# Kernel tuning notes

Measured on AMD Instinct MI355X. Metric: run time of the kernel, lower is better.

Reference implementation:

```python
import jax, jax.numpy as jnp
import numpy as np
from jax import lax

PAD_ID = 0
V, E = 100000, 300          # word vocab / embedding dim
VC, EC, C = 100, 50, 100    # char vocab / char emb dim / char conv channels
H, L = 256, 17              # lstm hidden / n_labels
B, S, LC = 32, 128, 50


def _conv1d(x, w, b):
    # x [B, Cin, T], w [Cout, Cin, K] -> valid conv
    y = lax.conv_general_dilated(x, w, window_strides=(1,), padding='VALID',
                                 dimension_numbers=('NCH', 'OIH', 'NCH'))
    return y + b[None, :, None]


def _lstm_dir(x_sbd, w_ih, w_hh, b, h0, c0):
    # x_sbd [S,B,D]; PyTorch gate order i,f,g,o
    def step(carry, x_t):
        h, c = carry
        g = x_t @ w_ih.T + h @ w_hh.T + b
        i, f, gg, o = jnp.split(g, 4, axis=-1)
        c = jax.nn.sigmoid(f) * c + jax.nn.sigmoid(i) * jnp.tanh(gg)
        h = jax.nn.sigmoid(o) * jnp.tanh(c)
        return (h, c), h
    _, hs = lax.scan(step, (h0, c0), x_sbd)
    return hs  # [S,B,H]


def _emissions(x, x_char, word_emb, char_emb,
               conv1_w, conv1_b, conv2_w, conv2_b, conv3_w, conv3_b,
               w_ih_f, w_hh_f, b_f, w_ih_b, w_hh_b, b_b, h0, c0, fc_w, fc_b):
    emb = word_emb[x]                                   # [B,S,E]
    ce = char_emb[x_char].transpose(0, 2, 1)            # [B,EC,LC]
    ce = jax.nn.relu(_conv1d(ce, conv1_w, conv1_b))
    ce = jax.nn.relu(_conv1d(ce, conv2_w, conv2_b))
    ce = jax.nn.relu(_conv1d(ce, conv3_w, conv3_b))
    pooled = ce.max(axis=2)                             # [B,C] (max over time)
    char_rep = jnp.broadcast_to(pooled[:, None, :], (emb.shape[0], emb.shape[1], pooled.shape[1]))
    xin = jnp.concatenate([emb, char_rep], axis=2)      # [B,S,E+C]
    xs = xin.transpose(1, 0, 2)                         # [S,B,D]
    hf = _lstm_dir(xs, w_ih_f, w_hh_f, b_f, h0[0], c0[0])
    hb = _lstm_dir(xs[::-1], w_ih_b, w_hh_b, b_b, h0[1], c0[1])[::-1]
    hcat = jnp.concatenate([hf, hb], axis=-1).transpose(1, 0, 2)  # [B,S,2H]
    em = hcat @ fc_w.T + fc_b                           # [B,S,L]
    return jax.nn.softmax(em, axis=1)                   # faithful: softmax over seq dim


def _viterbi(emissions, mask, start_t, trans, end_t):
    # emissions [B,S,L], mask [B,S]
    em = emissions.transpose(1, 0, 2)                   # [S,B,L]
    m = mask.T                                          # [S,B]
    score0 = start_t[None, :] + em[0]                   # [B,L]

    def fwd(score, inp):
        e_t, m_t = inp
        cand = score[:, :, None] + trans[None] + e_t[:, None, :]  # [B,L,L]
        nscore = cand.max(axis=1)
        idx = cand.argmax(axis=1).astype(jnp.int32)
        score = jnp.where(m_t[:, None] > 0, nscore, score)
        return score, idx

    score, hist = lax.scan(fwd, score0, (em[1:], m[1:]))  # hist [S-1,B,L]
    score = score + end_t[None, :]
    last = jnp.argmax(score, axis=-1).astype(jnp.int32)   # [B]

    def back(cur, inp):
        h_t, m_t = inp
        prev = jnp.take_along_axis(h_t, cur[:, None], axis=1)[:, 0]
        cur = jnp.where(m_t > 0, prev, cur)
        return cur, cur

    _, tags_rev = lax.scan(back, last, (hist[::-1], m[1:][::-1]))
    tags = jnp.concatenate([tags_rev[::-1], last[None]], axis=0)  # [S,B]
    return tags.T                                                 # [B,S]


def setup_inputs() -> dict:
    key = jax.random.key(0)
    ks = jax.random.split(key, 24)
    f = lambda i, shape, s=0.1: (jax.random.normal(ks[i], shape, dtype=jnp.float32) * s)
    inp = {
        'x': jax.random.randint(ks[0], (B, S), 1, V),          # no PAD -> mask all ones
        'x_char': jax.random.randint(ks[1], (B, LC), 1, VC),
        'word_emb': f(2, (V, E), 1.0),
        'char_emb': f(3, (VC, EC), 1.0).at[PAD_ID].set(0.0),
        'conv1_w': f(4, (C, EC, 3)), 'conv1_b': f(5, (C,)),
        'conv2_w': f(6, (C, C, 4)), 'conv2_b': f(7, (C,)),
        'conv3_w': f(8, (C, C, 5)), 'conv3_b': f(9, (C,)),
        'w_ih_f': f(10, (4 * H, E + C)), 'w_hh_f': f(11, (4 * H, H)), 'b_f': f(12, (4 * H,)),
        'w_ih_b': f(13, (4 * H, E + C)), 'w_hh_b': f(14, (4 * H, H)), 'b_b': f(15, (4 * H,)),
        'h0': f(16, (2, B, H), 1.0), 'c0': f(17, (2, B, H), 1.0),
        'fc_w': f(18, (L, 2 * H)), 'fc_b': f(19, (L,)),
        'start_t': f(20, (L,)), 'trans': f(21, (L, L)), 'end_t': f(22, (L,)),
    }
    return inp


def reference(x, x_char, word_emb, char_emb, conv1_w, conv1_b, conv2_w, conv2_b,
              conv3_w, conv3_b, w_ih_f, w_hh_f, b_f, w_ih_b, w_hh_b, b_b,
              h0, c0, fc_w, fc_b, start_t, trans, end_t):
    mask = (x != PAD_ID).astype(jnp.float32)
    em = _emissions(x, x_char, word_emb, char_emb, conv1_w, conv1_b, conv2_w, conv2_b,
                    conv3_w, conv3_b, w_ih_f, w_hh_f, b_f, w_ih_b, w_hh_b, b_b,
                    h0, c0, fc_w, fc_b)
    return _viterbi(em, mask, start_t, trans, end_t)
```

## Files before the change

### kernel.cpp

```cpp
#include <hip/hip_runtime.h>
#include <cmath>

#define B_   32
#define S_   128
#define E_   300
#define C_   100
#define EC_  50
#define LC_  50
#define H_   256
#define G4_  1024
#define L_   17
#define DHID_ 400
#define SLAB_ 8192
#define SENT2_ 0x7E007E00u
#define KP_   208

#define MRB_HINIT 0
#define MNB_HINIT 256
#define MRB_PW    256
#define MNB_PW    64
#define MRB_PB1   320
#define MNB_PB1   128
#define NBLK_MISC 448

#define TRB_FC   0
#define TNB_FC   128
#define TRB_SMV  128
#define TNB_SMV  32
#define NBLK_TAIL 160
#define F_EM  6

typedef _Float16 half8 __attribute__((ext_vector_type(8)));
typedef float f32x4 __attribute__((ext_vector_type(4)));
typedef unsigned long long ull;
struct __align__(16) U2 { ull x, y; };

__device__ __forceinline__ unsigned pack_split(float v) {
  _Float16 hi = (fabsf(v) >= 6.104e-5f) ? (_Float16)v : (_Float16)0.0f;
  float hif = (float)hi;
  _Float16 lo = (_Float16)((v - hif) * 2048.0f);
  return (unsigned)__builtin_bit_cast(unsigned short, hi)
       | ((unsigned)__builtin_bit_cast(unsigned short, lo) << 16);
}

__device__ __forceinline__ void flag_signal(int* f) {
  __syncthreads();
  if (threadIdx.x == 0)
    __hip_atomic_fetch_add(f, 1, __ATOMIC_RELEASE, __HIP_MEMORY_SCOPE_AGENT);
}
__device__ __forceinline__ void flag_wait(const int* f, int target) {
  while (__hip_atomic_load(f, __ATOMIC_ACQUIRE, __HIP_MEMORY_SCOPE_AGENT) < target)
    __builtin_amdgcn_s_sleep(16);
}

__global__ void k_misc(const int* __restrict__ x, const float* __restrict__ word_emb,
                       const float* __restrict__ h0,
                       const float* __restrict__ w_ih_f, const float* __restrict__ w_ih_b,
                       unsigned* __restrict__ hfrag,
                       unsigned* __restrict__ apH, unsigned* __restrict__ apL,
                       unsigned* __restrict__ bpH, unsigned* __restrict__ bpL,
                       int* __restrict__ flags) {
  const int bid = blockIdx.x;
  const int tid = threadIdx.x;
  if (bid == 0 && tid < 128) flags[tid] = 0;

  if (bid < MRB_PW) {
    const int g0 = bid * 256 + tid;
    const int nth = MNB_HINIT * 256;
    const int htot = 2 * (S_ + 1) * SLAB_;
    for (int idx = g0; idx < htot; idx += nth) {
      int sd = idx / SLAB_;
      int within = idx % SLAB_;
      int t = sd % (S_ + 1), d = sd / (S_ + 1);
      if (t != 0) { hfrag[idx] = SENT2_; continue; }
      int m8 = within & 7;
      int lane = (within >> 3) & 63;
      int q = within >> 9;
      int Kt = q & 7, Nt = q >> 3;
      int m = m8 & 3, isLo = m8 >> 2;
      int k0 = Kt * 32 + (lane >> 4) * 8 + 2 * m;
      int b = Nt * 16 + (lane & 15);
      unsigned p0 = pack_split(h0[((size_t)d * B_ + b) * H_ + k0]);
      unsigned p1 = pack_split(h0[((size_t)d * B_ + b) * H_ + k0 + 1]);
      unsigned hiw = (p0 & 0xFFFFu) | (p1 << 16);
      unsigned low = (p0 >> 16) | (p1 & 0xFFFF0000u);
      hfrag[idx] = isLo ? low : hiw;
    }
    return;
  } else if (bid < MRB_PB1) {
    const int q = bid - MRB_PW;
    const int total = 2 * G4_ * KP_;
    for (int idx = q * 256 + tid; idx < total; idx += MNB_PW * 256) {
      int d = idx / (G4_ * KP_);
      int rem = idx % (G4_ * KP_);
      int j = rem / KP_, k2 = rem % KP_;
      const float* w2 = d ? w_ih_b : w_ih_f;
      float v0 = 0.f, v1 = 0.f;
      if (k2 < 200) { v0 = w2[(size_t)j * DHID_ + 2 * k2]; v1 = w2[(size_t)j * DHID_ + 2 * k2 + 1]; }
      unsigned p0 = pack_split(v0), p1 = pack_split(v1);
      apH[idx] = (p0 & 0xFFFFu) | (p1 << 16);
      apL[idx] = (p0 >> 16) | (p1 & 0xFFFF0000u);
    }
    return;
  } else {
    const int q = bid - MRB_PB1;
    if (tid < KP_) {
      int k2 = tid;
      for (int rr = 0; rr < 32; ++rr) {
        int r = q * 32 + rr;
        int t2 = r >> 5, b2 = r & 31;
        if (k2 < 150) {
          const float* e2 = word_emb + (size_t)x[b2 * S_ + t2] * E_;
          unsigned p0 = pack_split(e2[2 * k2]), p1 = pack_split(e2[2 * k2 + 1]);
          bpH[(size_t)r * KP_ + k2] = (p0 & 0xFFFFu) | (p1 << 16);
          bpL[(size_t)r * KP_ + k2] = (p0 >> 16) | (p1 & 0xFFFF0000u);
        } else if (k2 >= 200) {
          bpH[(size_t)r * KP_ + k2] = 0u;
          bpL[(size_t)r * KP_ + k2] = 0u;
        }
      }
    }
    return;
  }
}

__global__ void k_conv1(const int* __restrict__ x_char, const float* __restrict__ char_emb,
                        const float* __restrict__ w1, const float* __restrict__ b1,
                        float* __restrict__ out1) {
  int b = blockIdx.x;
  int ot = blockIdx.y;
  __shared__ float ce[EC_ * 52];
  __shared__ float wl[50 * 150];
  __shared__ int ids[LC_];
  int tid = threadIdx.x;
  if (tid < LC_) ids[tid] = x_char[b * LC_ + tid];
  __syncthreads();
  for (int idx = tid; idx < LC_ * EC_; idx += 256) {
    int t = idx / EC_, ec = idx % EC_;
    ce[ec * 52 + t] = char_emb[ids[t] * EC_ + ec];
  }
  int obase = ot * 50;
  for (int idx = tid; idx < 50 * 150; idx += 256)
    wl[idx] = w1[obase * 150 + idx];
  __syncthreads();
  for (int idx = tid; idx < 50 * 48; idx += 256) {
    int o = idx / 48, t = idx % 48;
    float acc = b1[obase + o];
    const float* wr = &wl[o * 150];
    for (int c = 0; c < EC_; ++c) {
      const float* ip = &ce[c * 52 + t];
      acc += wr[c * 3 + 0] * ip[0] + wr[c * 3 + 1] * ip[1] + wr[c * 3 + 2] * ip[2];
    }
    out1[((size_t)b * C_ + obase + o) * 48 + t] = fmaxf(acc, 0.0f);
  }
}

__global__ void k_conv2(const float* __restrict__ in, const float* __restrict__ w2,
                        const float* __restrict__ b2, float* __restrict__ out2) {
  int b = blockIdx.x, ot = blockIdx.y;
  __shared__ float il[C_ * 48];
  __shared__ float wl[25 * 400];
  int tid = threadIdx.x;
  for (int idx = tid; idx < C_ * 48; idx += 256) il[idx] = in[(size_t)b * C_ * 48 + idx];
  int obase = ot * 25;
  for (int idx = tid; idx < 25 * 400; idx += 256) wl[idx] = w2[obase * 400 + idx];
  __syncthreads();
  for (int idx = tid; idx < 25 * 45; idx += 256) {
    int o = idx / 45, t = idx % 45;
    float acc = b2[obase + o];
    const float* wr = &wl[o * 400];
    for (int c = 0; c < C_; ++c) {
      const float* ip = &il[c * 48 + t];
      acc += wr[c * 4 + 0] * ip[0] + wr[c * 4 + 1] * ip[1] +
             wr[c * 4 + 2] * ip[2] + wr[c * 4 + 3] * ip[3];
    }
    out2[((size_t)b * C_ + obase + o) * 45 + t] = fmaxf(acc, 0.0f);
  }
}

__global__ void k_conv3(const float* __restrict__ in, const float* __restrict__ w3,
                        const float* __restrict__ b3, float* __restrict__ pooled) {
  int b = blockIdx.x, ot = blockIdx.y;
  __shared__ float il[C_ * 45];
  __shared__ float wl[20 * 500];
  __shared__ float o3[20 * 44];
  int tid = threadIdx.x;
  for (int idx = tid; idx < C_ * 45; idx += 256) il[idx] = in[(size_t)b * C_ * 45 + idx];
  int obase = ot * 20;
  for (int idx = tid; idx < 20 * 500; idx += 256) wl[idx] = w3[obase * 500 + idx];
  __syncthreads();
  for (int idx = tid; idx < 20 * 41; idx += 256) {
    int o = idx / 41, t = idx % 41;
    float acc = b3[obase + o];
    const float* wr = &wl[o * 500];
    for (int c = 0; c < C_; ++c) {
      const float* ip = &il[c * 45 + t];
      acc += wr[c * 5 + 0] * ip[0] + wr[c * 5 + 1] * ip[1] + wr[c * 5 + 2] * ip[2] +
             wr[c * 5 + 3] * ip[3] + wr[c * 5 + 4] * ip[4];
    }
    o3[o * 44 + t] = fmaxf(acc, 0.0f);
  }
  __syncthreads();
  if (tid < 20) {
    float m = o3[tid * 44];
    for (int t = 1; t < 41; ++t) m = fmaxf(m, o3[tid * 44 + t]);
    pooled[b * C_ + obase + tid] = m;
  }
}

__global__ void k_pb2(const float* __restrict__ pooled,
                      unsigned* __restrict__ bpH, unsigned* __restrict__ bpL) {
  const int q = blockIdx.x;
  const int k2 = threadIdx.x;
  if (k2 < 150 || k2 >= 200) return;
  for (int rr = 0; rr < 32; ++rr) {
    int r = q * 32 + rr;
    int b2 = r & 31;
    float v0 = pooled[b2 * C_ + 2 * k2 - 300];
    float v1 = pooled[b2 * C_ + 2 * k2 - 299];
    unsigned p0 = pack_split(v0), p1 = pack_split(v1);
    bpH[(size_t)r * KP_ + k2] = (p0 & 0xFFFFu) | (p1 << 16);
    bpL[(size_t)r * KP_ + k2] = (p0 >> 16) | (p1 & 0xFFFF0000u);
  }
}

__global__ __launch_bounds__(256) void k_gemm(
    const unsigned* __restrict__ apH, const unsigned* __restrict__ apL,
    const unsigned* __restrict__ bpH, const unsigned* __restrict__ bpL,
    const float* __restrict__ b_f, const float* __restrict__ b_b,
    float* __restrict__ gi) {
  const int jt = blockIdx.x, rt = blockIdx.y, d = blockIdx.z;
  const int j0 = jt * 128, r0 = rt * 128;
  const int tid = threadIdx.x;
  const int w = tid >> 6, l = tid & 63;
  const int lx = l & 15, lq = l >> 4;

  __shared__ unsigned aH[2048], aL[2048], bH[2048], bL[2048];

  f32x4 acch[2][8], accl[2][8];
#pragma unroll
  for (int mt = 0; mt < 2; ++mt)
#pragma unroll
    for (int nt = 0; nt < 8; ++nt) {
      f32x4 z = {0.f, 0.f, 0.f, 0.f};
      acch[mt][nt] = z; accl[mt][nt] = z;
    }

  const int jr = tid >> 1, hh = tid & 1;
  const int q_st = jr >> 4, lane_lo = jr & 15;
  const unsigned* arH = apH + ((size_t)(d * G4_ + j0 + jr)) * KP_ + hh * 8;
  const unsigned* arL = apL + ((size_t)(d * G4_ + j0 + jr)) * KP_ + hh * 8;
  const unsigned* brH = bpH + ((size_t)(r0 + jr)) * KP_ + hh * 8;
  const unsigned* brL = bpL + ((size_t)(r0 + jr)) * KP_ + hh * 8;
  const int w0 = (q_st * 64 + lane_lo + 32 * hh) * 4;
  const int w1 = (q_st * 64 + lane_lo + 32 * hh + 16) * 4;

  for (int Kt = 0; Kt < 13; ++Kt) {
    uint4 a0 = *(const uint4*)(arH + Kt * 16);
    uint4 a1 = *(const uint4*)(arH + Kt * 16 + 4);
    uint4 c0v = *(const uint4*)(arL + Kt * 16);
    uint4 c1v = *(const uint4*)(arL + Kt * 16 + 4);
    uint4 e0 = *(const uint4*)(brH + Kt * 16);
    uint4 e1 = *(const uint4*)(brH + Kt * 16 + 4);
    uint4 f0 = *(const uint4*)(brL + Kt * 16);
    uint4 f1 = *(const uint4*)(brL + Kt * 16 + 4);
    *(uint4*)&aH[w0] = a0; *(uint4*)&aH[w1] = a1;
    *(uint4*)&aL[w0] = c0v; *(uint4*)&aL[w1] = c1v;
    *(uint4*)&bH[w0] = e0; *(uint4*)&bH[w1] = e1;
    *(uint4*)&bL[w0] = f0; *(uint4*)&bL[w1] = f1;
    __syncthreads();

    union u4h { uint4 u; half8 h; };
    u4h AH0, AH1, AL0, AL1;
    AH0.u = *(const uint4*)&aH[((2 * w + 0) * 64 + l) * 4];
    AH1.u = *(const uint4*)&aH[((2 * w + 1) * 64 + l) * 4];
    AL0.u = *(const uint4*)&aL[((2 * w + 0) * 64 + l) * 4];
    AL1.u = *(const uint4*)&aL[((2 * w + 1) * 64 + l) * 4];
#pragma unroll
    for (int nt = 0; nt < 8; ++nt) {
      u4h BHn, BLn;
      BHn.u = *(const uint4*)&bH[(nt * 64 + l) * 4];
      BLn.u = *(const uint4*)&bL[(nt * 64 + l) * 4];
      acch[0][nt] = __builtin_amdgcn_mfma_f32_16x16x32_f16(AH0.h, BHn.h, acch[0][nt], 0, 0, 0);
      accl[0][nt] = __builtin_amdgcn_mfma_f32_16x16x32_f16(AH0.h, BLn.h, accl[0][nt], 0, 0, 0);
      accl[0][nt] = __builtin_amdgcn_mfma_f32_16x16x32_f16(AL0.h, BHn.h, accl[0][nt], 0, 0, 0);
      acch[1][nt] = __builtin_amdgcn_mfma_f32_16x16x32_f16(AH1.h, BHn.h, acch[1][nt], 0, 0, 0);
      accl[1][nt] = __builtin_amdgcn_mfma_f32_16x16x32_f16(AH1.h, BLn.h, accl[1][nt], 0, 0, 0);
      accl[1][nt] = __builtin_amdgcn_mfma_f32_16x16x32_f16(AL1.h, BHn.h, accl[1][nt], 0, 0, 0);
    }
    __syncthreads();
  }

  const float* bias = d ? b_b : b_f;
  const float inv2048 = 1.0f / 2048.0f;
#pragma unroll
  for (int mt = 0; mt < 2; ++mt) {
#pragma unroll
    for (int nt = 0; nt < 8; ++nt) {
      int rr = r0 + nt * 16 + lx;
      int tt = rr >> 5, bb = rr & 31;
      float* dst = gi + ((size_t)(d * S_ + tt) * G4_) * B_ + bb;
#pragma unroll
      for (int r4 = 0; r4 < 4; ++r4) {
        int j = j0 + (2 * w + mt) * 16 + lq * 4 + r4;
        dst[(size_t)j * B_] = acch[mt][nt][r4] + accl[mt][nt][r4] * inv2048 + bias[j];
      }
    }
  }
}

__global__ __launch_bounds__(256, 1) void k_lstm(
    const float* __restrict__ w_hh_f, const float* __restrict__ w_hh_b,
    const float* __restrict__ c0, const float* __restrict__ gi,
    float* __restrict__ hbuf, unsigned* __restrict__ hfrag) {
  const int iblk = blockIdx.x;
  const int d = blockIdx.y;
  const int Ktown = iblk >> 1;
  const int half = iblk & 1;
  const float* whh = d ? w_hh_b : w_hh_f;
  const int tid = threadIdx.x;
  const int w = tid >> 6;
  const int l = tid & 63;
  const int lx = l & 15, lq = l >> 4;
  const int u0 = iblk * 16;

  __shared__ ull slh[2048];
  __shared__ ull sll[2048];
  __shared__ float gl[4 * 16 * 33];
  __shared__ unsigned ps[2 * 576];

  half8 whi[8], wlo[8];
#pragma unroll
  for (int Kt = 0; Kt < 8; ++Kt) {
    int row = w * H_ + u0 + lx;
    int kk0 = Kt * 32 + lq * 8;
    const float* src = whh + (size_t)row * H_ + kk0;
    float4 f0 = *(const float4*)src;
    float4 f1 = *(const float4*)(src + 4);
    float wv[8] = {f0.x, f0.y, f0.z, f0.w, f1.x, f1.y, f1.z, f1.w};
    union { unsigned short s2[8]; half8 h; } HI, LO;
#pragma unroll
    for (int j = 0; j < 8; ++j) {
      float v = wv[j];
      _Float16 hi = (fabsf(v) >= 6.104e-5f) ? (_Float16)v : (_Float16)0.0f;
      float hif = (float)hi;
      _Float16 lo = (_Float16)((v - hif) * 2048.0f);
      HI.s2[j] = __builtin_bit_cast(unsigned short, hi);
      LO.s2[j] = __builtin_bit_cast(unsigned short, lo);
    }
    whi[Kt] = HI.h;
    wlo[Kt] = LO.h;
  }

  const int bc = tid & 31, cw = tid >> 5;
  float creg[2];
#pragma unroll
  for (int cu = 0; cu < 2; ++cu)
    creg[cu] = c0[((size_t)d * B_ + bc) * H_ + u0 + cu * 8 + cw];

  const int pNt = bc >> 4;
  const int pm = cw >> 1;
  const bool phi = (cw & 1) == 0;
  const int plane = bc & 15;
  const float inv2048 = 1.0f / 2048.0f;

  for (int t = 0; t < S_; ++t) {
    int torig = d ? (S_ - 1 - t) : t;

    f32x4 acch[2], accl[2];
    {
      const float* gbase = gi + ((size_t)(d * S_ + torig) * G4_) * B_;
#pragma unroll
      for (int Nt = 0; Nt < 2; ++Nt) {
        f32x4 v;
#pragma unroll
        for (int r = 0; r < 4; ++r) {
          int j = w * H_ + u0 + lq * 4 + r;
          v[r] = gbase[(size_t)j * B_ + Nt * 16 + lx];
        }
        acch[Nt] = v;
        f32x4 z = {0.f, 0.f, 0.f, 0.f};
        accl[Nt] = z;
      }
    }

    const ull* hp = (const ull*)(hfrag + (size_t)(d * (S_ + 1) + t) * SLAB_);
    ull pv[4][4];
#pragma unroll
    for (int c = 0; c < 4; ++c) {
      size_t base = ((size_t)(w * 4 + c) * 64 + l) * 4;
#pragma unroll
      for (int j = 0; j < 4; ++j)
        pv[c][j] = __hip_atomic_load(&hp[base + j], __ATOMIC_RELAXED,
                                     __HIP_MEMORY_SCOPE_AGENT);
    }
    for (;;) {
      bool pending = false;
#pragma unroll
      for (int c = 0; c < 4; ++c)
#pragma unroll
        for (int j = 0; j < 4; ++j)
          pending |= ((unsigned)pv[c][j] == SENT2_) |
                     ((unsigned)(pv[c][j] >> 32) == SENT2_);
      if (!pending) break;
#pragma unroll
      for (int c = 0; c < 4; ++c) {
        size_t base = ((size_t)(w * 4 + c) * 64 + l) * 4;
#pragma unroll
        for (int j = 0; j < 4; ++j)
          pv[c][j] = __hip_atomic_load(&hp[base + j], __ATOMIC_RELAXED,
                                       __HIP_MEMORY_SCOPE_AGENT);
      }
    }
#pragma unroll
    for (int c = 0; c < 4; ++c) {
      int idx = ((w * 4 + c) * 64 + l) * 2;
      U2 vh; vh.x = pv[c][0]; vh.y = pv[c][1];
      U2 vl; vl.x = pv[c][2]; vl.y = pv[c][3];
      *(U2*)&slh[idx] = vh;
      *(U2*)&sll[idx] = vl;
    }
    __syncthreads();

#pragma unroll
    for (int Kt = 0; Kt < 8; ++Kt) {
      half8 Bhi[2], Blo[2];
#pragma unroll
      for (int Nt = 0; Nt < 2; ++Nt) {
        int idx = ((Nt * 8 + Kt) * 64 + l) * 2;
        union { U2 u; half8 h; } UH, UL;
        UH.u = *(const U2*)&slh[idx];
        UL.u = *(const U2*)&sll[idx];
        Bhi[Nt] = UH.h;
        Blo[Nt] = UL.h;
      }
#pragma unroll
      for (int Nt = 0; Nt < 2; ++Nt) {
        acch[Nt] = __builtin_amdgcn_mfma_f32_16x16x32_f16(whi[Kt], Bhi[Nt], acch[Nt], 0, 0, 0);
        accl[Nt] = __builtin_amdgcn_mfma_f32_16x16x32_f16(whi[Kt], Blo[Nt], accl[Nt], 0, 0, 0);
        accl[Nt] = __builtin_amdgcn_mfma_f32_16x16x32_f16(wlo[Kt], Bhi[Nt], accl[Nt], 0, 0, 0);
      }
    }

#pragma unroll
    for (int Nt = 0; Nt < 2; ++Nt)
#pragma unroll
      for (int r = 0; r < 4; ++r) {
        int ul = lq * 4 + r;
        gl[(w * 16 + ul) * 33 + Nt * 16 + lx] = acch[Nt][r] + accl[Nt][r] * inv2048;
      }
    __syncthreads();

    float hreg[2];
#pragma unroll
    for (int cu = 0; cu < 2; ++cu) {
      int u = cu * 8 + cw;
      float g_i = gl[(0 * 16 + u) * 33 + bc];
      float g_f = gl[(1 * 16 + u) * 33 + bc];
      float g_g = gl[(2 * 16 + u) * 33 + bc];
      float g_o = gl[(3 * 16 + u) * 33 + bc];
      float si = 1.f / (1.f + __expf(-g_i));
      float sf = 1.f / (1.f + __expf(-g_f));
      float so = 1.f / (1.f + __expf(-g_o));
      float tg = 1.f - 2.f / (__expf(2.f * g_g) + 1.f);
      float cn = sf * creg[cu] + si * tg;
      float tc = 1.f - 2.f / (__expf(2.f * cn) + 1.f);
      float hn = so * tc;
      creg[cu] = cn;
      hreg[cu] = hn;
      unsigned me = pack_split(hn);
      unsigned pa = (unsigned)__shfl_xor((int)me, 32, 64);
      unsigned je = (cw & 1) ? pa : me;
      unsigned jo = (cw & 1) ? me : pa;
      unsigned hiw = (je & 0xFFFFu) | (jo << 16);
      unsigned low = (je >> 16) | (jo & 0xFFFF0000u);
      int lane2g = ((half * 2 + cu) << 4) | plane;
      int m8 = phi ? pm : (4 + pm);
      ps[pNt * 576 + lane2g * 9 + m8] = phi ? hiw : low;
    }
    __syncthreads();

    {
      ull* slab64 = (ull*)(hfrag + (size_t)(d * (S_ + 1) + t + 1) * SLAB_);
      int Nt = tid >> 7;
      int r = tid & 127;
      int lane2g = half * 32 + (r >> 2);
      int m2 = r & 3;
      unsigned a = ps[Nt * 576 + lane2g * 9 + 2 * m2];
      unsigned b2 = ps[Nt * 576 + lane2g * 9 + 2 * m2 + 1];
      ull v = (ull)a | ((ull)b2 << 32);
      __hip_atomic_store(&slab64[(size_t)(Nt * 8 + Ktown) * 256 + (size_t)half * 128 + r], v,
                         __ATOMIC_RELAXED, __HIP_MEMORY_SCOPE_AGENT);
      float* hb = hbuf + (size_t)(d * (S_ + 1) + t + 1) * (H_ * B_) + u0 * B_;
      hb[0 * 256 + tid] = hreg[0];
      hb[1 * 256 + tid] = hreg[1];
    }
  }
}

__global__ __launch_bounds__(256) void k_tail(
    const int* __restrict__ x, const float* __restrict__ hbuf,
    const float* __restrict__ fc_w, const float* __restrict__ fc_b,
    const float* __restrict__ start_t, const float* __restrict__ trans,
    const float* __restrict__ end_t,
    float* __restrict__ em, int* __restrict__ flags, int* __restrict__ out) {
  const int bid = blockIdx.x;
  union SMemTail {
    struct { float wT[512 * 18]; float psum[256 * 18]; } fc;
    struct { float e[S_ * L_]; float tr[L_ * L_]; float sc[2][L_];
             int hist[(S_ - 1) * L_]; int tags[S_]; } smv;
  };
  __shared__ SMemTail sm;

  if (bid < TRB_SMV) {
    const int s = bid;
    const int tid = threadIdx.x;
    float* wT = sm.fc.wT;
    float* psum = sm.fc.psum;
    for (int i = tid; i < L_ * 512; i += 256) {
      int l2 = i / 512, k = i % 512;
      wT[k * 18 + l2] = fc_w[i];
    }
    __syncthreads();
    const int b2 = tid & 31, kq = tid >> 5;
    const float* hf = hbuf + (size_t)(s + 1) * (H_ * B_);
    const float* hbk = hbuf + (size_t)(S_ + 1 + (S_ - s)) * (H_ * B_);
    float acc[L_];
#pragma unroll
    for (int l2 = 0; l2 < L_; ++l2) acc[l2] = 0.f;
    for (int i = 0; i < 64; ++i) {
      int k = kq * 64 + i;
      float hv = (k < 256) ? hf[k * 32 + b2] : hbk[(k - 256) * 32 + b2];
      const float* wr = &wT[k * 18];
#pragma unroll
      for (int l2 = 0; l2 < L_; ++l2) acc[l2] = fmaf(hv, wr[l2], acc[l2]);
    }
#pragma unroll
    for (int l2 = 0; l2 < L_; ++l2) psum[tid * 18 + l2] = acc[l2];
    __syncthreads();
    for (int idx = tid; idx < B_ * L_; idx += 256) {
      int bb2 = idx & 31, l2 = idx >> 5;
      float sum = fc_b[l2];
      for (int q2 = 0; q2 < 8; ++q2) sum += psum[(q2 * 32 + bb2) * 18 + l2];
      em[((size_t)bb2 * S_ + s) * L_ + l2] = sum;
    }
    flag_signal(&flags[F_EM]);
    return;
  } else {
    const int bb = bid - TRB_SMV;
    const int tid = threadIdx.x;
    float* e = sm.smv.e;
    float* tr = sm.smv.tr;
    auto sc = sm.smv.sc;
    int* hist = sm.smv.hist;
    int* tags = sm.smv.tags;

    if (tid == 0) flag_wait(&flags[F_EM], TNB_FC);
    __syncthreads();
    for (int i = tid; i < S_ * L_; i += 256) e[i] = em[(size_t)bb * S_ * L_ + i];
    for (int i = tid; i < L_ * L_; i += 256) tr[i] = trans[i];
    __syncthreads();
    if (tid < L_) {
      int l2 = tid;
      float m = -INFINITY;
      for (int s2 = 0; s2 < S_; ++s2) m = fmaxf(m, e[s2 * L_ + l2]);
      float sum2 = 0.f;
      for (int s2 = 0; s2 < S_; ++s2) {
        float ex = expf(e[s2 * L_ + l2] - m);
        e[s2 * L_ + l2] = ex;
        sum2 += ex;
      }
      for (int s2 = 0; s2 < S_; ++s2) e[s2 * L_ + l2] = e[s2 * L_ + l2] / sum2;
    }
    __syncthreads();
    if (tid < L_) sc[0][tid] = start_t[tid] + e[tid];
    __syncthreads();
    int cbuf = 0;
    for (int t2 = 1; t2 < S_; ++t2) {
      if (tid < L_) {
        int j2 = tid;
        float evv = e[t2 * L_ + j2];
        float best = -INFINITY;
        int arg = 0;
        for (int i = 0; i < L_; ++i) {
          float v = (sc[cbuf][i] + tr[i * L_ + j2]) + evv;
          if (v > best) { best = v; arg = i; }
        }
        int maskt = (x[bb * S_ + t2] != 0);
        sc[cbuf ^ 1][j2] = maskt ? best : sc[cbuf][j2];
        hist[(t2 - 1) * L_ + j2] = arg;
      }
      __syncthreads();
      cbuf ^= 1;
    }
    if (tid == 0) {
      float best = -INFINITY;
      int last = 0;
      for (int j2 = 0; j2 < L_; ++j2) {
        float v = sc[cbuf][j2] + end_t[j2];
        if (v > best) { best = v; last = j2; }
      }
      int cur = last;
      tags[S_ - 1] = cur;
      for (int p = S_ - 2; p >= 0; --p) {
        if (x[bb * S_ + p + 1] != 0) cur = hist[p * L_ + cur];
        tags[p] = cur;
      }
    }
    __syncthreads();
    for (int s2 = tid; s2 < S_; s2 += 256) out[bb * S_ + s2] = tags[s2];
    return;
  }
}

extern "C" void kernel_launch(void* const* d_in, const int* in_sizes, int n_in,
                              void* d_out, int out_size, void* d_ws, size_t ws_size,
                              hipStream_t stream) {
  const int* x        = (const int*)d_in[0];
  const int* x_char   = (const int*)d_in[1];
  const float* word_emb = (const float*)d_in[2];
  const float* char_emb = (const float*)d_in[3];
  const float* conv1_w = (const float*)d_in[4];
  const float* conv1_b = (const float*)d_in[5];
  const float* conv2_w = (const float*)d_in[6];
  const float* conv2_b = (const float*)d_in[7];
  const float* conv3_w = (const float*)d_in[8];
  const float* conv3_b = (const float*)d_in[9];
  const float* w_ih_f = (const float*)d_in[10];
  const float* w_hh_f = (const float*)d_in[11];
  const float* b_f    = (const float*)d_in[12];
  const float* w_ih_b = (const float*)d_in[13];
  const float* w_hh_b = (const float*)d_in[14];
  const float* b_b    = (const float*)d_in[15];
  const float* h0     = (const float*)d_in[16];
  const float* c0     = (const float*)d_in[17];
  const float* fc_w   = (const float*)d_in[18];
  const float* fc_b   = (const float*)d_in[19];
  const float* start_t = (const float*)d_in[20];
  const float* trans  = (const float*)d_in[21];
  const float* end_t  = (const float*)d_in[22];
  int* out = (int*)d_out;

  char* ws = (char*)d_ws;
  auto alloc = [&](size_t bytes) -> char* {
    char* p = ws;
    ws += (bytes + 1023) & ~(size_t)1023;
    return p;
  };
  float* pooled  = (float*)alloc(sizeof(float) * B_ * C_);
  float* gi      = (float*)alloc(sizeof(float) * 2 * S_ * G4_ * B_);
  float* hbuf    = (float*)alloc(sizeof(float) * 2 * (S_ + 1) * H_ * B_);
  unsigned* hfrag = (unsigned*)alloc(sizeof(unsigned) * 2 * (S_ + 1) * SLAB_);
  unsigned* apH  = (unsigned*)alloc(sizeof(unsigned) * 2 * G4_ * KP_);
  unsigned* apL  = (unsigned*)alloc(sizeof(unsigned) * 2 * G4_ * KP_);
  unsigned* bpH  = (unsigned*)alloc(sizeof(unsigned) * 4096 * KP_);
  unsigned* bpL  = (unsigned*)alloc(sizeof(unsigned) * 4096 * KP_);
  float* out1    = (float*)alloc(sizeof(float) * B_ * C_ * 48);
  float* out2    = (float*)alloc(sizeof(float) * B_ * C_ * 45);
  float* em      = (float*)alloc(sizeof(float) * B_ * S_ * L_);
  int* flags     = (int*)alloc(sizeof(int) * 128);

  k_misc<<<NBLK_MISC, 256, 0, stream>>>(x, word_emb, h0, w_ih_f, w_ih_b,
                                        hfrag, apH, apL, bpH, bpL, flags);
  k_conv1<<<dim3(32, 2), 256, 0, stream>>>(x_char, char_emb, conv1_w, conv1_b, out1);
  k_conv2<<<dim3(32, 4), 256, 0, stream>>>(out1, conv2_w, conv2_b, out2);
  k_conv3<<<dim3(32, 5), 256, 0, stream>>>(out2, conv3_w, conv3_b, pooled);
  k_pb2<<<128, 256, 0, stream>>>(pooled, bpH, bpL);
  k_gemm<<<dim3(8, 32, 2), 256, 0, stream>>>(apH, apL, bpH, bpL, b_f, b_b, gi);
  k_lstm<<<dim3(16, 2), 256, 0, stream>>>(w_hh_f, w_hh_b, c0, gi, hbuf, hfrag);
  k_tail<<<NBLK_TAIL, 256, 0, stream>>>(
      x, hbuf, fc_w, fc_b, start_t, trans, end_t, em, flags, out);
}
```

Baseline: 876.4 us.

## Fuse preprocessing, char convs, input GEMM and LSTM into one persistent kernel

Merges the packing, three char-conv stages, the input-projection GEMM and the LSTM recurrence into a single persistent kernel. Worker blocks pull tasks from atomic work queues and signal per-stage completion counters. The LSTM blocks wait on per-row-tile GEMM flags, so the recurrence can start before the whole input projection is done. The GEMM walks time tiles in order (reversed for the backward direction) to feed the recurrence early. The aim is to remove launch gaps and serialization between stages. The cost is spin-wait synchronization, a union of shared memory that may lower occupancy, and a risk of deadlock if not all blocks are co-resident.

```diff
diff --git a/kernel.cpp b/kernel.cpp
--- a/kernel.cpp
+++ b/kernel.cpp
@@ -15,20 +15,39 @@
 #define SENT2_ 0x7E007E00u
 #define KP_   208
 
-#define MRB_HINIT 0
-#define MNB_HINIT 256
-#define MRB_PW    256
-#define MNB_PW    64
-#define MRB_PB1   320
-#define MNB_PB1   128
-#define NBLK_MISC 448
+#define NB_LSTM   32
+#define NBLK_MEGA 256
+#define NTILE_G   512
+#define NIT_PW    64
+#define NIT_PB    128
+#define NIT_C1    64
+#define NIT_C2    128
+#define NIT_C3    160
 
 #define TRB_FC   0
 #define TNB_FC   128
 #define TRB_SMV  128
 #define TNB_SMV  32
 #define NBLK_TAIL 160
-#define F_EM  6
+
+#define F_HF   0
+#define D_PW   1
+#define D_PBE  2
+#define D_C1   3
+#define D_C2   4
+#define D_C3   5
+#define D_PB   6
+#define F_EM   7
+#define FG(d, rt) (8 + (d) * 32 + (rt))
+#define Q_PW   72
+#define Q_PB1  73
+#define Q_C1   74
+#define Q_C2   75
+#define Q_C3   76
+#define Q_PB2  77
+#define Q_G    78
+#define FLG(i)    ((i) * 32)
+#define NFLAGS_   (80 * 32)
 
 typedef _Float16 half8 __attribute__((ext_vector_type(8)));
 typedef float f32x4 __attribute__((ext_vector_type(4)));
@@ -50,359 +69,151 @@
 }
 __device__ __forceinline__ void flag_wait(const int* f, int target) {
   while (__hip_atomic_load(f, __ATOMIC_ACQUIRE, __HIP_MEMORY_SCOPE_AGENT) < target)
-    __builtin_amdgcn_s_sleep(16);
+    __builtin_amdgcn_s_sleep(8);
 }
 
-__global__ void k_misc(const int* __restrict__ x, const float* __restrict__ word_emb,
-                       const float* __restrict__ h0,
-                       const float* __restrict__ w_ih_f, const float* __restrict__ w_ih_b,
-                       unsigned* __restrict__ hfrag,
-                       unsigned* __restrict__ apH, unsigned* __restrict__ apL,
-                       unsigned* __restrict__ bpH, unsigned* __restrict__ bpL,
-                       int* __restrict__ flags) {
+union SMemMega {
+  char pad[84 * 1024];
+  struct { unsigned aH[2048], aL[2048], bH[2048], bL[2048]; } gemm;
+  struct { ull slh[2048], sll[2048]; float gl[4 * 16 * 33]; unsigned ps[2 * 576]; } lstm;
+  struct { float ce[EC_ * 52]; float wl[50 * 150]; int ids[LC_]; } c1;
+  struct { float il[C_ * 48]; float wl[25 * 400]; } c2;
+  struct { float il[C_ * 45]; float wl[20 * 500]; float o3[20 * 44]; } c3;
+};
+
+__global__ __launch_bounds__(256) void k_mega(
+    const int* __restrict__ x, const int* __restrict__ x_char,
+    const float* __restrict__ word_emb, const float* __restrict__ char_emb,
+    const float* __restrict__ conv1_w, const float* __restrict__ conv1_b,
+    const float* __restrict__ conv2_w, const float* __restrict__ conv2_b,
+    const float* __restrict__ conv3_w, const float* __restrict__ conv3_b,
+    const float* __restrict__ w_ih_f, const float* __restrict__ w_ih_b,
+    const float* __restrict__ w_hh_f, const float* __restrict__ w_hh_b,
+    const float* __restrict__ b_f, const float* __restrict__ b_b,
+    const float* __restrict__ h0, const float* __restrict__ c0,
+    float* __restrict__ pooled, float* __restrict__ gi, float* __restrict__ hbuf,
+    unsigned* __restrict__ hfrag,
+    unsigned* __restrict__ apH, unsigned* __restrict__ apL,
+    unsigned* __restrict__ bpH, unsigned* __restrict__ bpL,
+    float* __restrict__ out1, float* __restrict__ out2,
+    int* __restrict__ flags) {
   const int bid = blockIdx.x;
   const int tid = threadIdx.x;
-  if (bid == 0 && tid < 128) flags[tid] = 0;
-
-  if (bid < MRB_PW) {
-    const int g0 = bid * 256 + tid;
-    const int nth = MNB_HINIT * 256;
-    const int htot = 2 * (S_ + 1) * SLAB_;
-    for (int idx = g0; idx < htot; idx += nth) {
-      int sd = idx / SLAB_;
-      int within = idx % SLAB_;
-      int t = sd % (S_ + 1), d = sd / (S_ + 1);
-      if (t != 0) { hfrag[idx] = SENT2_; continue; }
-      int m8 = within & 7;
-      int lane = (within >> 3) & 63;
-      int q = within >> 9;
-      int Kt = q & 7, Nt = q >> 3;
-      int m = m8 & 3, isLo = m8 >> 2;
-      int k0 = Kt * 32 + (lane >> 4) * 8 + 2 * m;
-      int b = Nt * 16 + (lane & 15);
-      unsigned p0 = pack_split(h0[((size_t)d * B_ + b) * H_ + k0]);
-      unsigned p1 = pack_split(h0[((size_t)d * B_ + b) * H_ + k0 + 1]);
-      unsigned hiw = (p0 & 0xFFFFu) | (p1 << 16);
-      unsigned low = (p0 >> 16) | (p1 & 0xFFFF0000u);
-      hfrag[idx] = isLo ? low : hiw;
-    }
-    return;
-  } else if (bid < MRB_PB1) {
-    const int q = bid - MRB_PW;
-    const int total = 2 * G4_ * KP_;
-    for (int idx = q * 256 + tid; idx < total; idx += MNB_PW * 256) {
-      int d = idx / (G4_ * KP_);
-      int rem = idx % (G4_ * KP_);
-      int j = rem / KP_, k2 = rem % KP_;
-      const float* w2 = d ? w_ih_b : w_ih_f;
-      float v0 = 0.f, v1 = 0.f;
-      if (k2 < 200) { v0 = w2[(size_t)j * DHID_ + 2 * k2]; v1 = w2[(size_t)j * DHID_ + 2 * k2 + 1]; }
-      unsigned p0 = pack_split(v0), p1 = pack_split(v1);
-      apH[idx] = (p0 & 0xFFFFu) | (p1 << 16);
-      apL[idx] = (p0 >> 16) | (p1 & 0xFFFF0000u);
-    }
-    return;
-  } else {
-    const int q = bid - MRB_PB1;
-    if (tid < KP_) {
-      int k2 = tid;
-      for (int rr = 0; rr < 32; ++rr) {
-        int r = q * 32 + rr;
-        int t2 = r >> 5, b2 = r & 31;
-        if (k2 < 150) {
-          const float* e2 = word_emb + (size_t)x[b2 * S_ + t2] * E_;
-          unsigned p0 = pack_split(e2[2 * k2]), p1 = pack_split(e2[2 * k2 + 1]);
-          bpH[(size_t)r * KP_ + k2] = (p0 & 0xFFFFu) | (p1 << 16);
-          bpL[(size_t)r * KP_ + k2] = (p0 >> 16) | (p1 & 0xFFFF0000u);
-        } else if (k2 >= 200) {
-          bpH[(size_t)r * KP_ + k2] = 0u;
-          bpL[(size_t)r * KP_ + k2] = 0u;
-        }
-      }
-    }
-    return;
-  }
-}
-
-__global__ void k_conv1(const int* __restrict__ x_char, const float* __restrict__ char_emb,
-                        const float* __restrict__ w1, const float* __restrict__ b1,
-                        float* __restrict__ out1) {
-  int b = blockIdx.x;
-  int ot = blockIdx.y;
-  __shared__ float ce[EC_ * 52];
-  __shared__ float wl[50 * 150];
-  __shared__ int ids[LC_];
-  int tid = threadIdx.x;
-  if (tid < LC_) ids[tid] = x_char[b * LC_ + tid];
-  __syncthreads();
-  for (int idx = tid; idx < LC_ * EC_; idx += 256) {
-    int t = idx / EC_, ec = idx % EC_;
-    ce[ec * 52 + t] = char_emb[ids[t] * EC_ + ec];
-  }
-  int obase = ot * 50;
-  for (int idx = tid; idx < 50 * 150; idx += 256)
-    wl[idx] = w1[obase * 150 + idx];
-  __syncthreads();
-  for (int idx = tid; idx < 50 * 48; idx += 256) {
-    int o = idx / 48, t = idx % 48;
-    float acc = b1[obase + o];
-    const float* wr = &wl[o * 150];
-    for (int c = 0; c < EC_; ++c) {
-      const float* ip = &ce[c * 52 + t];
-      acc += wr[c * 3 + 0] * ip[0] + wr[c * 3 + 1] * ip[1] + wr[c * 3 + 2] * ip[2];
-    }
-    out1[((size_t)b * C_ + obase + o) * 48 + t] = fmaxf(acc, 0.0f);
-  }
-}
-
-__global__ void k_conv2(const float* __restrict__ in, const float* __restrict__ w2,
-                        const float* __restrict__ b2, float* __restrict__ out2) {
-  int b = blockIdx.x, ot = blockIdx.y;
-  __shared__ float il[C_ * 48];
-  __shared__ float wl[25 * 400];
-  int tid = threadIdx.x;
-  for (int idx = tid; idx < C_ * 48; idx += 256) il[idx] = in[(size_t)b * C_ * 48 + idx];
-  int obase = ot * 25;
-  for (int idx = tid; idx < 25 * 400; idx += 256) wl[idx] = w2[obase * 400 + idx];
-  __syncthreads();
-  for (int idx = tid; idx < 25 * 45; idx += 256) {
-    int o = idx / 45, t = idx % 45;
-    float acc = b2[obase + o];
-    const float* wr = &wl[o * 400];
-    for (int c = 0; c < C_; ++c) {
-      const float* ip = &il[c * 48 + t];
-      acc += wr[c * 4 + 0] * ip[0] + wr[c * 4 + 1] * ip[1] +
-             wr[c * 4 + 2] * ip[2] + wr[c * 4 + 3] * ip[3];
-    }
-    out2[((size_t)b * C_ + obase + o) * 45 + t] = fmaxf(acc, 0.0f);
-  }
-}
-
-__global__ void k_conv3(const float* __restrict__ in, const float* __restrict__ w3,
-                        const float* __restrict__ b3, float* __restrict__ pooled) {
-  int b = blockIdx.x, ot = blockIdx.y;
-  __shared__ float il[C_ * 45];
-  __shared__ float wl[20 * 500];
-  __shared__ float o3[20 * 44];
-  int tid = threadIdx.x;
-  for (int idx = tid; idx < C_ * 45; idx += 256) il[idx] = in[(size_t)b * C_ * 45 + idx];
-  int obase = ot * 20;
-  for (int idx = tid; idx < 20 * 500; idx += 256) wl[idx] = w3[obase * 500 + idx];
-  __syncthreads();
-  for (int idx = tid; idx < 20 * 41; idx += 256) {
-    int o = idx / 41, t = idx % 41;
-    float acc = b3[obase + o];
-    const float* wr = &wl[o * 500];
-    for (int c = 0; c < C_; ++c) {
-      const float* ip = &il[c * 45 + t];
-      acc += wr[c * 5 + 0] * ip[0] + wr[c * 5 + 1] * ip[1] + wr[c * 5 + 2] * ip[2] +
-             wr[c * 5 + 3] * ip[3] + wr[c * 5 + 4] * ip[4];
-    }
-    o3[o * 44 + t] = fmaxf(acc, 0.0f);
-  }
-  __syncthreads();
-  if (tid < 20) {
-    float m = o3[tid * 44];
-    for (int t = 1; t < 41; ++t) m = fmaxf(m, o3[tid * 44 + t]);
-    pooled[b * C_ + obase + tid] = m;
-  }
-}
-
-__global__ void k_pb2(const float* __restrict__ pooled,
-                      unsigned* __restrict__ bpH, unsigned* __restrict__ bpL) {
-  const int q = blockIdx.x;
-  const int k2 = threadIdx.x;
-  if (k2 < 150 || k2 >= 200) return;
-  for (int rr = 0; rr < 32; ++rr) {
-    int r = q * 32 + rr;
-    int b2 = r & 31;
-    float v0 = pooled[b2 * C_ + 2 * k2 - 300];
-    float v1 = pooled[b2 * C_ + 2 * k2 - 299];
-    unsigned p0 = pack_split(v0), p1 = pack_split(v1);
-    bpH[(size_t)r * KP_ + k2] = (p0 & 0xFFFFu) | (p1 << 16);
-    bpL[(size_t)r * KP_ + k2] = (p0 >> 16) | (p1 & 0xFFFF0000u);
-  }
-}
-
-__global__ __launch_bounds__(256) void k_gemm(
-    const unsigned* __restrict__ apH, const unsigned* __restrict__ apL,
-    const unsigned* __restrict__ bpH, const unsigned* __restrict__ bpL,
-    const float* __restrict__ b_f, const float* __restrict__ b_b,
-    float* __restrict__ gi) {
-  const int jt = blockIdx.x, rt = blockIdx.y, d = blockIdx.z;
-  const int j0 = jt * 128, r0 = rt * 128;
-  const int tid = threadIdx.x;
-  const int w = tid >> 6, l = tid & 63;
-  const int lx = l & 15, lq = l >> 4;
-
-  __shared__ unsigned aH[2048], aL[2048], bH[2048], bL[2048];
-
-  f32x4 acch[2][8], accl[2][8];
-#pragma unroll
-  for (int mt = 0; mt < 2; ++mt)
-#pragma unroll
-    for (int nt = 0; nt < 8; ++nt) {
-      f32x4 z = {0.f, 0.f, 0.f, 0.f};
-      acch[mt][nt] = z; accl[mt][nt] = z;
-    }
-
-  const int jr = tid >> 1, hh = tid & 1;
-  const int q_st = jr >> 4, lane_lo = jr & 15;
-  const unsigned* arH = apH + ((size_t)(d * G4_ + j0 + jr)) * KP_ + hh * 8;
-  const unsigned* arL = apL + ((size_t)(d * G4_ + j0 + jr)) * KP_ + hh * 8;
-  const unsigned* brH = bpH + ((size_t)(r0 + jr)) * KP_ + hh * 8;
-  const unsigned* brL = bpL + ((size_t)(r0 + jr)) * KP_ + hh * 8;
-  const int w0 = (q_st * 64 + lane_lo + 32 * hh) * 4;
-  const int w1 = (q_st * 64 + lane_lo + 32 * hh + 16) * 4;
-
-  for (int Kt = 0; Kt < 13; ++Kt) {
-    uint4 a0 = *(const uint4*)(arH + Kt * 16);
-    uint4 a1 = *(const uint4*)(arH + Kt * 16 + 4);
-    uint4 c0v = *(const uint4*)(arL + Kt * 16);
-    uint4 c1v = *(const uint4*)(arL + Kt * 16 + 4);
-    uint4 e0 = *(const uint4*)(brH + Kt * 16);
-    uint4 e1 = *(const uint4*)(brH + Kt * 16 + 4);
-    uint4 f0 = *(const uint4*)(brL + Kt * 16);
-    uint4 f1 = *(const uint4*)(brL + Kt * 16 + 4);
-    *(uint4*)&aH[w0] = a0; *(uint4*)&aH[w1] = a1;
-    *(uint4*)&aL[w0] = c0v; *(uint4*)&aL[w1] = c1v;
-    *(uint4*)&bH[w0] = e0; *(uint4*)&bH[w1] = e1;
-    *(uint4*)&bL[w0] = f0; *(uint4*)&bL[w1] = f1;
-    __syncthreads();
-
-    union u4h { uint4 u; half8 h; };
-    u4h AH0, AH1, AL0, AL1;
-    AH0.u = *(const uint4*)&aH[((2 * w + 0) * 64 + l) * 4];
-    AH1.u = *(const uint4*)&aH[((2 * w + 1) * 64 + l) * 4];
-    AL0.u = *(const uint4*)&aL[((2 * w + 0) * 64 + l) * 4];
-    AL1.u = *(const uint4*)&aL[((2 * w + 1) * 64 + l) * 4];
-#pragma unroll
-    for (int nt = 0; nt < 8; ++nt) {
-      u4h BHn, BLn;
-      BHn.u = *(const uint4*)&bH[(nt * 64 + l) * 4];
-      BLn.u = *(const uint4*)&bL[(nt * 64 + l) * 4];
-      acch[0][nt] = __builtin_amdgcn_mfma_f32_16x16x32_f16(AH0.h, BHn.h, acch[0][nt], 0, 0, 0);
-      accl[0][nt] = __builtin_amdgcn_mfma_f32_16x16x32_f16(AH0.h, BLn.h, accl[0][nt], 0, 0, 0);
-      accl[0][nt] = __builtin_amdgcn_mfma_f32_16x16x32_f16(AL0.h, BHn.h, accl[0][nt], 0, 0, 0);
-      acch[1][nt] = __builtin_amdgcn_mfma_f32_16x16x32_f16(AH1.h, BHn.h, acch[1][nt], 0, 0, 0);
-      accl[1][nt] = __builtin_amdgcn_mfma_f32_16x16x32_f16(AH1.h, BLn.h, accl[1][nt], 0, 0, 0);
-      accl[1][nt] = __builtin_amdgcn_mfma_f32_16x16x32_f16(AL1.h, BHn.h, accl[1][nt], 0, 0, 0);
-    }
-    __syncthreads();
-  }
-
-  const float* bias = d ? b_b : b_f;
-  const float inv2048 = 1.0f / 2048.0f;
-#pragma unroll
-  for (int mt = 0; mt < 2; ++mt) {
-#pragma unroll
-    for (int nt = 0; nt < 8; ++nt) {
-      int rr = r0 + nt * 16 + lx;
-      int tt = rr >> 5, bb = rr & 31;
-      float* dst = gi + ((size_t)(d * S_ + tt) * G4_) * B_ + bb;
-#pragma unroll
-      for (int r4 = 0; r4 < 4; ++r4) {
-        int j = j0 + (2 * w + mt) * 16 + lq * 4 + r4;
-        dst[(size_t)j * B_] = acch[mt][nt][r4] + accl[mt][nt][r4] * inv2048 + bias[j];
-      }
-    }
-  }
-}
-
-__global__ __launch_bounds__(256, 1) void k_lstm(
-    const float* __restrict__ w_hh_f, const float* __restrict__ w_hh_b,
-    const float* __restrict__ c0, const float* __restrict__ gi,
-    float* __restrict__ hbuf, unsigned* __restrict__ hfrag) {
-  const int iblk = blockIdx.x;
-  const int d = blockIdx.y;
-  const int Ktown = iblk >> 1;
-  const int half = iblk & 1;
-  const float* whh = d ? w_hh_b : w_hh_f;
-  const int tid = threadIdx.x;
-  const int w = tid >> 6;
-  const int l = tid & 63;
-  const int lx = l & 15, lq = l >> 4;
-  const int u0 = iblk * 16;
-
-  __shared__ ull slh[2048];
-  __shared__ ull sll[2048];
-  __shared__ float gl[4 * 16 * 33];
-  __shared__ unsigned ps[2 * 576];
-
-  half8 whi[8], wlo[8];
-#pragma unroll
-  for (int Kt = 0; Kt < 8; ++Kt) {
-    int row = w * H_ + u0 + lx;
-    int kk0 = Kt * 32 + lq * 8;
-    const float* src = whh + (size_t)row * H_ + kk0;
-    float4 f0 = *(const float4*)src;
-    float4 f1 = *(const float4*)(src + 4);
-    float wv[8] = {f0.x, f0.y, f0.z, f0.w, f1.x, f1.y, f1.z, f1.w};
-    union { unsigned short s2[8]; half8 h; } HI, LO;
-#pragma unroll
-    for (int j = 0; j < 8; ++j) {
-      float v = wv[j];
-      _Float16 hi = (fabsf(v) >= 6.104e-5f) ? (_Float16)v : (_Float16)0.0f;
-      float hif = (float)hi;
-      _Float16 lo = (_Float16)((v - hif) * 2048.0f);
-      HI.s2[j] = __builtin_bit_cast(unsigned short, hi);
-      LO.s2[j] = __builtin_bit_cast(unsigned short, lo);
-    }
-    whi[Kt] = HI.h;
-    wlo[Kt] = LO.h;
-  }
-
-  const int bc = tid & 31, cw = tid >> 5;
-  float creg[2];
-#pragma unroll
-  for (int cu = 0; cu < 2; ++cu)
-    creg[cu] = c0[((size_t)d * B_ + bc) * H_ + u0 + cu * 8 + cw];
-
-  const int pNt = bc >> 4;
-  const int pm = cw >> 1;
-  const bool phi = (cw & 1) == 0;
-  const int plane = bc & 15;
-  const float inv2048 = 1.0f / 2048.0f;
-
-  for (int t = 0; t < S_; ++t) {
-    int torig = d ? (S_ - 1 - t) : t;
-
-    f32x4 acch[2], accl[2];
+  __shared__ SMemMega sm;
+  __shared__ int curq;
+
+  if (bid < NB_LSTM) {
+    const int d = bid >> 4;
+    const int iblk = bid & 15;
+    const int Ktown = iblk >> 1;
+    const int half = iblk & 1;
+    const float* whh = d ? w_hh_b : w_hh_f;
+
     {
-      const float* gbase = gi + ((size_t)(d * S_ + torig) * G4_) * B_;
-#pragma unroll
-      for (int Nt = 0; Nt < 2; ++Nt) {
-        f32x4 v;
-#pragma unroll
-        for (int r = 0; r < 4; ++r) {
-          int j = w * H_ + u0 + lq * 4 + r;
-          v[r] = gbase[(size_t)j * B_ + Nt * 16 + lx];
-        }
-        acch[Nt] = v;
-        f32x4 z = {0.f, 0.f, 0.f, 0.f};
-        accl[Nt] = z;
-      }
-    }
-
-    const ull* hp = (const ull*)(hfrag + (size_t)(d * (S_ + 1) + t) * SLAB_);
-    ull pv[4][4];
-#pragma unroll
-    for (int c = 0; c < 4; ++c) {
-      size_t base = ((size_t)(w * 4 + c) * 64 + l) * 4;
-#pragma unroll
-      for (int j = 0; j < 4; ++j)
-        pv[c][j] = __hip_atomic_load(&hp[base + j], __ATOMIC_RELAXED,
-                                     __HIP_MEMORY_SCOPE_AGENT);
-    }
-    for (;;) {
-      bool pending = false;
-#pragma unroll
-      for (int c = 0; c < 4; ++c)
-#pragma unroll
-        for (int j = 0; j < 4; ++j)
-          pending |= ((unsigned)pv[c][j] == SENT2_) |
-                     ((unsigned)(pv[c][j] >> 32) == SENT2_);
-      if (!pending) break;
+      const int items = (S_ + 1) * 512;
+      for (int idx2 = tid; idx2 < items; idx2 += 256) {
+        int t = idx2 >> 9;
+        int within = idx2 & 511;
+        int Nt = within >> 8;
+        int rem = within & 255;
+        int lane = half * 32 + (rem >> 3);
+        int m8 = rem & 7;
+        size_t u = (size_t)(d * (S_ + 1) + t) * SLAB_ +
+                   (((size_t)(Nt * 8 + Ktown) * 64 + lane) * 8 + m8);
+        if (t != 0) { hfrag[u] = SENT2_; continue; }
+        int m = m8 & 3, isLo = m8 >> 2;
+        int k0 = Ktown * 32 + (lane >> 4) * 8 + 2 * m;
+        int b = Nt * 16 + (lane & 15);
+        unsigned p0 = pack_split(h0[((size_t)d * B_ + b) * H_ + k0]);
+        unsigned p1 = pack_split(h0[((size_t)d * B_ + b) * H_ + k0 + 1]);
+        unsigned hiw = (p0 & 0xFFFFu) | (p1 << 16);
+        unsigned low = (p0 >> 16) | (p1 & 0xFFFF0000u);
+        hfrag[u] = isLo ? low : hiw;
+      }
+      flag_signal(&flags[FLG(F_HF)]);
+      flag_wait(&flags[FLG(F_HF)], NB_LSTM);
+      __syncthreads();
+    }
+
+    const int w = tid >> 6;
+    const int l = tid & 63;
+    const int lx = l & 15, lq = l >> 4;
+    const int u0 = iblk * 16;
+
+    ull* slh = sm.lstm.slh;
+    ull* sll = sm.lstm.sll;
+    float* glb = sm.lstm.gl;
+    unsigned* ps = sm.lstm.ps;
+
+    half8 whi[8], wlo[8];
+#pragma unroll
+    for (int Kt = 0; Kt < 8; ++Kt) {
+      int row = w * H_ + u0 + lx;
+      int kk0 = Kt * 32 + lq * 8;
+      const float* src = whh + (size_t)row * H_ + kk0;
+      float4 f0 = *(const float4*)src;
+      float4 f1 = *(const float4*)(src + 4);
+      float wv[8] = {f0.x, f0.y, f0.z, f0.w, f1.x, f1.y, f1.z, f1.w};
+      union { unsigned short s2[8]; half8 h; } HI, LO;
+#pragma unroll
+      for (int j = 0; j < 8; ++j) {
+        float v = wv[j];
+        _Float16 hi = (fabsf(v) >= 6.104e-5f) ? (_Float16)v : (_Float16)0.0f;
+        float hif = (float)hi;
+        _Float16 lo = (_Float16)((v - hif) * 2048.0f);
+        HI.s2[j] = __builtin_bit_cast(unsigned short, hi);
+        LO.s2[j] = __builtin_bit_cast(unsigned short, lo);
+      }
+      whi[Kt] = HI.h;
+      wlo[Kt] = LO.h;
+    }
+
+    const int bc = tid & 31, cw = tid >> 5;
+    float creg[2];
+#pragma unroll
+    for (int cu = 0; cu < 2; ++cu)
+      creg[cu] = c0[((size_t)d * B_ + bc) * H_ + u0 + cu * 8 + cw];
+
+    const int pNt = bc >> 4;
+    const int pm = cw >> 1;
+    const bool phi = (cw & 1) == 0;
+    const int plane = bc & 15;
+    const float inv2048 = 1.0f / 2048.0f;
+
+    int rt_have = -1;
+    for (int t = 0; t < S_; ++t) {
+      int torig = d ? (S_ - 1 - t) : t;
+
+      int rt = torig >> 2;
+      if (rt != rt_have) {
+        if (tid == 0) {
+          const int* gf = &flags[FLG(FG(d, rt))];
+          while (__hip_atomic_load(gf, __ATOMIC_ACQUIRE, __HIP_MEMORY_SCOPE_AGENT) < 8)
+            __builtin_amdgcn_s_sleep(2);
+        }
+        __syncthreads();
+        rt_have = rt;
+      }
+
+      f32x4 acch[2], accl[2];
+      {
+        const float* gbase = gi + ((size_t)(d * S_ + torig) * G4_) * B_;
+#pragma unroll
+        for (int Nt = 0; Nt < 2; ++Nt) {
+          f32x4 v;
+#pragma unroll
+          for (int r = 0; r < 4; ++r) {
+            int j = w * H_ + u0 + lq * 4 + r;
+            v[r] = gbase[(size_t)j * B_ + Nt * 16 + lx];
+          }
+          acch[Nt] = v;
+          f32x4 z = {0.f, 0.f, 0.f, 0.f};
+          accl[Nt] = z;
+        }
+      }
+
+      const ull* hp = (const ull*)(hfrag + (size_t)(d * (S_ + 1) + t) * SLAB_);
+      ull pv[4][4];
 #pragma unroll
       for (int c = 0; c < 4; ++c) {
         size_t base = ((size_t)(w * 4 + c) * 64 + l) * 4;
@@ -411,90 +222,387 @@
           pv[c][j] = __hip_atomic_load(&hp[base + j], __ATOMIC_RELAXED,
                                        __HIP_MEMORY_SCOPE_AGENT);
       }
-    }
-#pragma unroll
-    for (int c = 0; c < 4; ++c) {
-      int idx = ((w * 4 + c) * 64 + l) * 2;
-      U2 vh; vh.x = pv[c][0]; vh.y = pv[c][1];
-      U2 vl; vl.x = pv[c][2]; vl.y = pv[c][3];
-      *(U2*)&slh[idx] = vh;
-      *(U2*)&sll[idx] = vl;
-    }
-    __syncthreads();
-
-#pragma unroll
-    for (int Kt = 0; Kt < 8; ++Kt) {
-      half8 Bhi[2], Blo[2];
-#pragma unroll
-      for (int Nt = 0; Nt < 2; ++Nt) {
-        int idx = ((Nt * 8 + Kt) * 64 + l) * 2;
-        union { U2 u; half8 h; } UH, UL;
-        UH.u = *(const U2*)&slh[idx];
-        UL.u = *(const U2*)&sll[idx];
-        Bhi[Nt] = UH.h;
-        Blo[Nt] = UL.h;
-      }
-#pragma unroll
-      for (int Nt = 0; Nt < 2; ++Nt) {
-        acch[Nt] = __builtin_amdgcn_mfma_f32_16x16x32_f16(whi[Kt], Bhi[Nt], acch[Nt], 0, 0, 0);
-        accl[Nt] = __builtin_amdgcn_mfma_f32_16x16x32_f16(whi[Kt], Blo[Nt], accl[Nt], 0, 0, 0);
-        accl[Nt] = __builtin_amdgcn_mfma_f32_16x16x32_f16(wlo[Kt], Bhi[Nt], accl[Nt], 0, 0, 0);
-      }
-    }
-
-#pragma unroll
-    for (int Nt = 0; Nt < 2; ++Nt)
-#pragma unroll
-      for (int r = 0; r < 4; ++r) {
-        int ul = lq * 4 + r;
-        gl[(w * 16 + ul) * 33 + Nt * 16 + lx] = acch[Nt][r] + accl[Nt][r] * inv2048;
-      }
-    __syncthreads();
-
-    float hreg[2];
-#pragma unroll
-    for (int cu = 0; cu < 2; ++cu) {
-      int u = cu * 8 + cw;
-      float g_i = gl[(0 * 16 + u) * 33 + bc];
-      float g_f = gl[(1 * 16 + u) * 33 + bc];
-      float g_g = gl[(2 * 16 + u) * 33 + bc];
-      float g_o = gl[(3 * 16 + u) * 33 + bc];
-      float si = 1.f / (1.f + __expf(-g_i));
-      float sf = 1.f / (1.f + __expf(-g_f));
-      float so = 1.f / (1.f + __expf(-g_o));
-      float tg = 1.f - 2.f / (__expf(2.f * g_g) + 1.f);
-      float cn = sf * creg[cu] + si * tg;
-      float tc = 1.f - 2.f / (__expf(2.f * cn) + 1.f);
-      float hn = so * tc;
-      creg[cu] = cn;
-      hreg[cu] = hn;
-      unsigned me = pack_split(hn);
-      unsigned pa = (unsigned)__shfl_xor((int)me, 32, 64);
-      unsigned je = (cw & 1) ? pa : me;
-      unsigned jo = (cw & 1) ? me : pa;
-      unsigned hiw = (je & 0xFFFFu) | (jo << 16);
-      unsigned low = (je >> 16) | (jo & 0xFFFF0000u);
-      int lane2g = ((half * 2 + cu) << 4) | plane;
-      int m8 = phi ? pm : (4 + pm);
-      ps[pNt * 576 + lane2g * 9 + m8] = phi ? hiw : low;
-    }
-    __syncthreads();
-
-    {
-      ull* slab64 = (ull*)(hfrag + (size_t)(d * (S_ + 1) + t + 1) * SLAB_);
-      int Nt = tid >> 7;
-      int r = tid & 127;
-      int lane2g = half * 32 + (r >> 2);
-      int m2 = r & 3;
-      unsigned a = ps[Nt * 576 + lane2g * 9 + 2 * m2];
-      unsigned b2 = ps[Nt * 576 + lane2g * 9 + 2 * m2 + 1];
-      ull v = (ull)a | ((ull)b2 << 32);
-      __hip_atomic_store(&slab64[(size_t)(Nt * 8 + Ktown) * 256 + (size_t)half * 128 + r], v,
-                         __ATOMIC_RELAXED, __HIP_MEMORY_SCOPE_AGENT);
-      float* hb = hbuf + (size_t)(d * (S_ + 1) + t + 1) * (H_ * B_) + u0 * B_;
-      hb[0 * 256 + tid] = hreg[0];
-      hb[1 * 256 + tid] = hreg[1];
-    }
+      for (;;) {
+        bool pending = false;
+#pragma unroll
+        for (int c = 0; c < 4; ++c)
+#pragma unroll
+          for (int j = 0; j < 4; ++j)
+            pending |= ((unsigned)pv[c][j] == SENT2_) |
+                       ((unsigned)(pv[c][j] >> 32) == SENT2_);
+        if (!pending) break;
+#pragma unroll
+        for (int c = 0; c < 4; ++c) {
+          size_t base = ((size_t)(w * 4 + c) * 64 + l) * 4;
+#pragma unroll
+          for (int j = 0; j < 4; ++j)
+            pv[c][j] = __hip_atomic_load(&hp[base + j], __ATOMIC_RELAXED,
+                                         __HIP_MEMORY_SCOPE_AGENT);
+        }
+      }
+#pragma unroll
+      for (int c = 0; c < 4; ++c) {
+        int idx = ((w * 4 + c) * 64 + l) * 2;
+        U2 vh; vh.x = pv[c][0]; vh.y = pv[c][1];
+        U2 vl; vl.x = pv[c][2]; vl.y = pv[c][3];
+        *(U2*)&slh[idx] = vh;
+        *(U2*)&sll[idx] = vl;
+      }
+      __syncthreads();
+
+#pragma unroll
+      for (int Kt = 0; Kt < 8; ++Kt) {
+        half8 Bhi[2], Blo[2];
+#pragma unroll
+        for (int Nt = 0; Nt < 2; ++Nt) {
+          int idx = ((Nt * 8 + Kt) * 64 + l) * 2;
+          union { U2 u; half8 h; } UH, UL;
+          UH.u = *(const U2*)&slh[idx];
+          UL.u = *(const U2*)&sll[idx];
+          Bhi[Nt] = UH.h;
+          Blo[Nt] = UL.h;
+        }
+#pragma unroll
+        for (int Nt = 0; Nt < 2; ++Nt) {
+          acch[Nt] = __builtin_amdgcn_mfma_f32_16x16x32_f16(whi[Kt], Bhi[Nt], acch[Nt], 0, 0, 0);
+          accl[Nt] = __builtin_amdgcn_mfma_f32_16x16x32_f16(whi[Kt], Blo[Nt], accl[Nt], 0, 0, 0);
+          accl[Nt] = __builtin_amdgcn_mfma_f32_16x16x32_f16(wlo[Kt], Bhi[Nt], accl[Nt], 0, 0, 0);
+        }
+      }
+
+#pragma unroll
+      for (int Nt = 0; Nt < 2; ++Nt)
+#pragma unroll
+        for (int r = 0; r < 4; ++r) {
+          int ul = lq * 4 + r;
+          glb[(w * 16 + ul) * 33 + Nt * 16 + lx] = acch[Nt][r] + accl[Nt][r] * inv2048;
+        }
+      __syncthreads();
+
+      float hreg[2];
+#pragma unroll
+      for (int cu = 0; cu < 2; ++cu) {
+        int u = cu * 8 + cw;
+        float g_i = glb[(0 * 16 + u) * 33 + bc];
+        float g_f = glb[(1 * 16 + u) * 33 + bc];
+        float g_g = glb[(2 * 16 + u) * 33 + bc];
+        float g_o = glb[(3 * 16 + u) * 33 + bc];
+        float si = 1.f / (1.f + __expf(-g_i));
+        float sf = 1.f / (1.f + __expf(-g_f));
+        float so = 1.f / (1.f + __expf(-g_o));
+        float tg = 1.f - 2.f / (__expf(2.f * g_g) + 1.f);
+        float cn = sf * creg[cu] + si * tg;
+        float tc = 1.f - 2.f / (__expf(2.f * cn) + 1.f);
+        float hn = so * tc;
+        creg[cu] = cn;
+        hreg[cu] = hn;
+        unsigned me = pack_split(hn);
+        unsigned pa = (unsigned)__shfl_xor((int)me, 32, 64);
+        unsigned je = (cw & 1) ? pa : me;
+        unsigned jo = (cw & 1) ? me : pa;
+        unsigned hiw = (je & 0xFFFFu) | (jo << 16);
+        unsigned low = (je >> 16) | (jo & 0xFFFF0000u);
+        int lane2g = ((half * 2 + cu) << 4) | plane;
+        int m8 = phi ? pm : (4 + pm);
+        ps[pNt * 576 + lane2g * 9 + m8] = phi ? hiw : low;
+      }
+      __syncthreads();
+
+      {
+        ull* slab64 = (ull*)(hfrag + (size_t)(d * (S_ + 1) + t + 1) * SLAB_);
+        int Nt = tid >> 7;
+        int r = tid & 127;
+        int lane2g = half * 32 + (r >> 2);
+        int m2 = r & 3;
+        unsigned a = ps[Nt * 576 + lane2g * 9 + 2 * m2];
+        unsigned b2 = ps[Nt * 576 + lane2g * 9 + 2 * m2 + 1];
+        ull v = (ull)a | ((ull)b2 << 32);
+        __hip_atomic_store(&slab64[(size_t)(Nt * 8 + Ktown) * 256 + (size_t)half * 128 + r], v,
+                           __ATOMIC_RELAXED, __HIP_MEMORY_SCOPE_AGENT);
+        float* hb = hbuf + (size_t)(d * (S_ + 1) + t + 1) * (H_ * B_) + u0 * B_;
+        hb[0 * 256 + tid] = hreg[0];
+        hb[1 * 256 + tid] = hreg[1];
+      }
+    }
+    return;
+  }
+
+  {
+    for (;;) {
+      __syncthreads();
+      if (tid == 0)
+        curq = __hip_atomic_fetch_add(&flags[FLG(Q_PW)], 1, __ATOMIC_RELAXED,
+                                      __HIP_MEMORY_SCOPE_AGENT);
+      __syncthreads();
+      const int q = curq;
+      if (q >= NIT_PW) break;
+      const int base = q * 6656;
+      for (int idx = base + tid; idx < base + 6656; idx += 256) {
+        int d = idx / (G4_ * KP_);
+        int rem = idx % (G4_ * KP_);
+        int j = rem / KP_, k2 = rem % KP_;
+        const float* w2 = d ? w_ih_b : w_ih_f;
+        float v0 = 0.f, v1 = 0.f;
+        if (k2 < 200) { v0 = w2[(size_t)j * DHID_ + 2 * k2]; v1 = w2[(size_t)j * DHID_ + 2 * k2 + 1]; }
+        unsigned p0 = pack_split(v0), p1 = pack_split(v1);
+        apH[idx] = (p0 & 0xFFFFu) | (p1 << 16);
+        apL[idx] = (p0 >> 16) | (p1 & 0xFFFF0000u);
+      }
+      flag_signal(&flags[FLG(D_PW)]);
+    }
+
+    for (;;) {
+      __syncthreads();
+      if (tid == 0)
+        curq = __hip_atomic_fetch_add(&flags[FLG(Q_PB1)], 1, __ATOMIC_RELAXED,
+                                      __HIP_MEMORY_SCOPE_AGENT);
+      __syncthreads();
+      const int q = curq;
+      if (q >= NIT_PB) break;
+      if (tid < KP_) {
+        int k2 = tid;
+        for (int rr = 0; rr < 32; ++rr) {
+          int r = q * 32 + rr;
+          int t2 = r >> 5, b2 = r & 31;
+          if (k2 < 150) {
+            const float* e2 = word_emb + (size_t)x[b2 * S_ + t2] * E_;
+            unsigned p0 = pack_split(e2[2 * k2]), p1 = pack_split(e2[2 * k2 + 1]);
+            bpH[(size_t)r * KP_ + k2] = (p0 & 0xFFFFu) | (p1 << 16);
+            bpL[(size_t)r * KP_ + k2] = (p0 >> 16) | (p1 & 0xFFFF0000u);
+          } else if (k2 >= 200) {
+            bpH[(size_t)r * KP_ + k2] = 0u;
+            bpL[(size_t)r * KP_ + k2] = 0u;
+          }
+        }
+      }
+      flag_signal(&flags[FLG(D_PBE)]);
+    }
+
+    for (;;) {
+      __syncthreads();
+      if (tid == 0)
+        curq = __hip_atomic_fetch_add(&flags[FLG(Q_C1)], 1, __ATOMIC_RELAXED,
+                                      __HIP_MEMORY_SCOPE_AGENT);
+      __syncthreads();
+      const int q = curq;
+      if (q >= NIT_C1) break;
+      const int b2 = q & 31, ot = q >> 5;
+      float* ce = sm.c1.ce;
+      float* wl = sm.c1.wl;
+      int* ids = sm.c1.ids;
+      if (tid < LC_) ids[tid] = x_char[b2 * LC_ + tid];
+      __syncthreads();
+      for (int idx = tid; idx < LC_ * EC_; idx += 256) {
+        int t2 = idx / EC_, ec = idx % EC_;
+        ce[ec * 52 + t2] = char_emb[ids[t2] * EC_ + ec];
+      }
+      int obase = ot * 50;
+      for (int idx = tid; idx < 50 * 150; idx += 256)
+        wl[idx] = conv1_w[obase * 150 + idx];
+      __syncthreads();
+      for (int idx = tid; idx < 50 * 48; idx += 256) {
+        int o = idx / 48, t2 = idx % 48;
+        float acc = conv1_b[obase + o];
+        const float* wr = &wl[o * 150];
+        for (int c = 0; c < EC_; ++c) {
+          const float* ip = &ce[c * 52 + t2];
+          acc += wr[c * 3 + 0] * ip[0] + wr[c * 3 + 1] * ip[1] + wr[c * 3 + 2] * ip[2];
+        }
+        out1[((size_t)b2 * C_ + obase + o) * 48 + t2] = fmaxf(acc, 0.0f);
+      }
+      flag_signal(&flags[FLG(D_C1)]);
+    }
+    flag_wait(&flags[FLG(D_C1)], NIT_C1);
+
+    for (;;) {
+      __syncthreads();
+      if (tid == 0)
+        curq = __hip_atomic_fetch_add(&flags[FLG(Q_C2)], 1, __ATOMIC_RELAXED,
+                                      __HIP_MEMORY_SCOPE_AGENT);
+      __syncthreads();
+      const int q = curq;
+      if (q >= NIT_C2) break;
+      const int b2 = q & 31, ot = q >> 5;
+      float* il = sm.c2.il;
+      float* wl = sm.c2.wl;
+      for (int idx = tid; idx < C_ * 48; idx += 256) il[idx] = out1[(size_t)b2 * C_ * 48 + idx];
+      int obase = ot * 25;
+      for (int idx = tid; idx < 25 * 400; idx += 256) wl[idx] = conv2_w[obase * 400 + idx];
+      __syncthreads();
+      for (int idx = tid; idx < 25 * 45; idx += 256) {
+        int o = idx / 45, t2 = idx % 45;
+        float acc = conv2_b[obase + o];
+        const float* wr = &wl[o * 400];
+        for (int c = 0; c < C_; ++c) {
+          const float* ip = &il[c * 48 + t2];
+          acc += wr[c * 4 + 0] * ip[0] + wr[c * 4 + 1] * ip[1] +
+                 wr[c * 4 + 2] * ip[2] + wr[c * 4 + 3] * ip[3];
+        }
+        out2[((size_t)b2 * C_ + obase + o) * 45 + t2] = fmaxf(acc, 0.0f);
+      }
+      flag_signal(&flags[FLG(D_C2)]);
+    }
+    flag_wait(&flags[FLG(D_C2)], NIT_C2);
+
+    for (;;) {
+      __syncthreads();
+      if (tid == 0)
+        curq = __hip_atomic_fetch_add(&flags[FLG(Q_C3)], 1, __ATOMIC_RELAXED,
+                                      __HIP_MEMORY_SCOPE_AGENT);
+      __syncthreads();
+      const int q = curq;
+      if (q >= NIT_C3) break;
+      const int b2 = q % 32, ot = q / 32;
+      float* il = sm.c3.il;
+      float* wl = sm.c3.wl;
+      float* o3 = sm.c3.o3;
+      for (int idx = tid; idx < C_ * 45; idx += 256) il[idx] = out2[(size_t)b2 * C_ * 45 + idx];
+      int obase = ot * 20;
+      for (int idx = tid; idx < 20 * 500; idx += 256) wl[idx] = conv3_w[obase * 500 + idx];
+      __syncthreads();
+      for (int idx = tid; idx < 20 * 41; idx += 256) {
+        int o = idx / 41, t2 = idx % 41;
+        float acc = conv3_b[obase + o];
+        const float* wr = &wl[o * 500];
+        for (int c = 0; c < C_; ++c) {
+          const float* ip = &il[c * 45 + t2];
+          acc += wr[c * 5 + 0] * ip[0] + wr[c * 5 + 1] * ip[1] + wr[c * 5 + 2] * ip[2] +
+                 wr[c * 5 + 3] * ip[3] + wr[c * 5 + 4] * ip[4];
+        }
+        o3[o * 44 + t2] = fmaxf(acc, 0.0f);
+      }
+      __syncthreads();
+      if (tid < 20) {
+        float m = o3[tid * 44];
+        for (int t2 = 1; t2 < 41; ++t2) m = fmaxf(m, o3[tid * 44 + t2]);
+        pooled[b2 * C_ + obase + tid] = m;
+      }
+      flag_signal(&flags[FLG(D_C3)]);
+    }
+    flag_wait(&flags[FLG(D_C3)], NIT_C3);
+
+    for (;;) {
+      __syncthreads();
+      if (tid == 0)
+        curq = __hip_atomic_fetch_add(&flags[FLG(Q_PB2)], 1, __ATOMIC_RELAXED,
+                                      __HIP_MEMORY_SCOPE_AGENT);
+      __syncthreads();
+      const int q = curq;
+      if (q >= NIT_PB) break;
+      if (tid >= 150 && tid < 200) {
+        int k2 = tid;
+        for (int rr = 0; rr < 32; ++rr) {
+          int r = q * 32 + rr;
+          int b2 = r & 31;
+          float v0 = pooled[b2 * C_ + 2 * k2 - 300];
+          float v1 = pooled[b2 * C_ + 2 * k2 - 299];
+          unsigned p0 = pack_split(v0), p1 = pack_split(v1);
+          bpH[(size_t)r * KP_ + k2] = (p0 & 0xFFFFu) | (p1 << 16);
+          bpL[(size_t)r * KP_ + k2] = (p0 >> 16) | (p1 & 0xFFFF0000u);
+        }
+      }
+      flag_signal(&flags[FLG(D_PB)]);
+    }
+    flag_wait(&flags[FLG(D_PB)], NIT_PB);
+    flag_wait(&flags[FLG(D_PW)], NIT_PW);
+    flag_wait(&flags[FLG(D_PBE)], NIT_PB);
+
+    const int w = tid >> 6, l = tid & 63;
+    const int lx = l & 15, lq = l >> 4;
+    const int jr = tid >> 1, hh = tid & 1;
+    const int q_st = jr >> 4, lane_lo = jr & 15;
+    const int w0 = (q_st * 64 + lane_lo + 32 * hh) * 4;
+    const int w1 = (q_st * 64 + lane_lo + 32 * hh + 16) * 4;
+    unsigned* aH = sm.gemm.aH;
+    unsigned* aL = sm.gemm.aL;
+    unsigned* bH = sm.gemm.bH;
+    unsigned* bL = sm.gemm.bL;
+
+    for (;;) {
+      __syncthreads();
+      if (tid == 0)
+        curq = __hip_atomic_fetch_add(&flags[FLG(Q_G)], 1, __ATOMIC_RELAXED,
+                                      __HIP_MEMORY_SCOPE_AGENT);
+      __syncthreads();
+      const int g = curq;
+      if (g >= NTILE_G) break;
+      const int d = g & 1;
+      const int jt = (g >> 1) & 7;
+      const int rtb = g >> 4;
+      const int rt = d ? (31 - rtb) : rtb;
+      const int j0 = jt * 128, r0 = rt * 128;
+
+      f32x4 acch[2][8], accl[2][8];
+#pragma unroll
+      for (int mt = 0; mt < 2; ++mt)
+#pragma unroll
+        for (int nt = 0; nt < 8; ++nt) {
+          f32x4 z = {0.f, 0.f, 0.f, 0.f};
+          acch[mt][nt] = z; accl[mt][nt] = z;
+        }
+
+      const unsigned* arH = apH + ((size_t)(d * G4_ + j0 + jr)) * KP_ + hh * 8;
+      const unsigned* arL = apL + ((size_t)(d * G4_ + j0 + jr)) * KP_ + hh * 8;
+      const unsigned* brH = bpH + ((size_t)(r0 + jr)) * KP_ + hh * 8;
+      const unsigned* brL = bpL + ((size_t)(r0 + jr)) * KP_ + hh * 8;
+
+      for (int Kt = 0; Kt < 13; ++Kt) {
+        uint4 a0 = *(const uint4*)(arH + Kt * 16);
+        uint4 a1 = *(const uint4*)(arH + Kt * 16 + 4);
+        uint4 c0v = *(const uint4*)(arL + Kt * 16);
+        uint4 c1v = *(const uint4*)(arL + Kt * 16 + 4);
+        uint4 e0 = *(const uint4*)(brH + Kt * 16);
+        uint4 e1 = *(const uint4*)(brH + Kt * 16 + 4);
+        uint4 f0 = *(const uint4*)(brL + Kt * 16);
+        uint4 f1 = *(const uint4*)(brL + Kt * 16 + 4);
+        *(uint4*)&aH[w0] = a0; *(uint4*)&aH[w1] = a1;
+        *(uint4*)&aL[w0] = c0v; *(uint4*)&aL[w1] = c1v;
+        *(uint4*)&bH[w0] = e0; *(uint4*)&bH[w1] = e1;
+        *(uint4*)&bL[w0] = f0; *(uint4*)&bL[w1] = f1;
+        __syncthreads();
+
+        union u4h { uint4 u; half8 h; };
+        u4h AH0, AH1, AL0, AL1;
+        AH0.u = *(const uint4*)&aH[((2 * w + 0) * 64 + l) * 4];
+        AH1.u = *(const uint4*)&aH[((2 * w + 1) * 64 + l) * 4];
+        AL0.u = *(const uint4*)&aL[((2 * w + 0) * 64 + l) * 4];
+        AL1.u = *(const uint4*)&aL[((2 * w + 1) * 64 + l) * 4];
+#pragma unroll
+        for (int nt = 0; nt < 8; ++nt) {
+          u4h BHn, BLn;
+          BHn.u = *(const uint4*)&bH[(nt * 64 + l) * 4];
+          BLn.u = *(const uint4*)&bL[(nt * 64 + l) * 4];
+          acch[0][nt] = __builtin_amdgcn_mfma_f32_16x16x32_f16(AH0.h, BHn.h, acch[0][nt], 0, 0, 0);
+          accl[0][nt] = __builtin_amdgcn_mfma_f32_16x16x32_f16(AH0.h, BLn.h, accl[0][nt], 0, 0, 0);
+          accl[0][nt] = __builtin_amdgcn_mfma_f32_16x16x32_f16(AL0.h, BHn.h, accl[0][nt], 0, 0, 0);
+          acch[1][nt] = __builtin_amdgcn_mfma_f32_16x16x32_f16(AH1.h, BHn.h, acch[1][nt], 0, 0, 0);
+          accl[1][nt] = __builtin_amdgcn_mfma_f32_16x16x32_f16(AH1.h, BLn.h, accl[1][nt], 0, 0, 0);
+          accl[1][nt] = __builtin_amdgcn_mfma_f32_16x16x32_f16(AL1.h, BHn.h, accl[1][nt], 0, 0, 0);
+        }
+        __syncthreads();
+      }
+
+      const float* bias = d ? b_b : b_f;
+      const float inv2048 = 1.0f / 2048.0f;
+#pragma unroll
+      for (int mt = 0; mt < 2; ++mt) {
+#pragma unroll
+        for (int nt = 0; nt < 8; ++nt) {
+          int rr = r0 + nt * 16 + lx;
+          int tt = rr >> 5, bb2 = rr & 31;
+          unsigned* dst = (unsigned*)gi + ((size_t)(d * S_ + tt) * G4_) * B_ + bb2;
+#pragma unroll
+          for (int r4 = 0; r4 < 4; ++r4) {
+            int j = j0 + (2 * w + mt) * 16 + lq * 4 + r4;
+            float vv = acch[mt][nt][r4] + accl[mt][nt][r4] * inv2048 + bias[j];
+            __hip_atomic_store(&dst[(size_t)j * B_], __builtin_bit_cast(unsigned, vv),
+                               __ATOMIC_RELAXED, __HIP_MEMORY_SCOPE_AGENT);
+          }
+        }
+      }
+      flag_signal(&flags[FLG(FG(d, rt))]);
+    }
+    return;
   }
 }
 
@@ -544,7 +652,7 @@
       for (int q2 = 0; q2 < 8; ++q2) sum += psum[(q2 * 32 + bb2) * 18 + l2];
       em[((size_t)bb2 * S_ + s) * L_ + l2] = sum;
     }
-    flag_signal(&flags[F_EM]);
+    flag_signal(&flags[FLG(F_EM)]);
     return;
   } else {
     const int bb = bid - TRB_SMV;
@@ -555,7 +663,7 @@
     int* hist = sm.smv.hist;
     int* tags = sm.smv.tags;
 
-    if (tid == 0) flag_wait(&flags[F_EM], TNB_FC);
+    if (tid == 0) flag_wait(&flags[FLG(F_EM)], TNB_FC);
     __syncthreads();
     for (int i = tid; i < S_ * L_; i += 256) e[i] = em[(size_t)bb * S_ * L_ + i];
     for (int i = tid; i < L_ * L_; i += 256) tr[i] = trans[i];
@@ -658,16 +766,14 @@
   float* out1    = (float*)alloc(sizeof(float) * B_ * C_ * 48);
   float* out2    = (float*)alloc(sizeof(float) * B_ * C_ * 45);
   float* em      = (float*)alloc(sizeof(float) * B_ * S_ * L_);
-  int* flags     = (int*)alloc(sizeof(int) * 128);
-
-  k_misc<<<NBLK_MISC, 256, 0, stream>>>(x, word_emb, h0, w_ih_f, w_ih_b,
-                                        hfrag, apH, apL, bpH, bpL, flags);
-  k_conv1<<<dim3(32, 2), 256, 0, stream>>>(x_char, char_emb, conv1_w, conv1_b, out1);
-  k_conv2<<<dim3(32, 4), 256, 0, stream>>>(out1, conv2_w, conv2_b, out2);
-  k_conv3<<<dim3(32, 5), 256, 0, stream>>>(out2, conv3_w, conv3_b, pooled);
-  k_pb2<<<128, 256, 0, stream>>>(pooled, bpH, bpL);
-  k_gemm<<<dim3(8, 32, 2), 256, 0, stream>>>(apH, apL, bpH, bpL, b_f, b_b, gi);
-  k_lstm<<<dim3(16, 2), 256, 0, stream>>>(w_hh_f, w_hh_b, c0, gi, hbuf, hfrag);
+  int* flags     = (int*)alloc(sizeof(int) * NFLAGS_);
+
+  hipMemsetAsync(flags, 0, sizeof(int) * NFLAGS_, stream);
+  k_mega<<<NBLK_MEGA, 256, 0, stream>>>(
+      x, x_char, word_emb, char_emb,
+      conv1_w, conv1_b, conv2_w, conv2_b, conv3_w, conv3_b,
+      w_ih_f, w_ih_b, w_hh_f, w_hh_b, b_f, b_b, h0, c0,
+      pooled, gi, hbuf, hfrag, apH, apL, bpH, bpL, out1, out2, flags);
   k_tail<<<NBLK_TAIL, 256, 0, stream>>>(
       x, hbuf, fc_w, fc_b, start_t, trans, end_t, em, flags, out);
 }
```

After: 971.4 us. 1.11x slower.
